# Optimization experiments

Measured on AMD Instinct MI355X. Metric: run time of the kernel, lower is better.

The kernel has to match this reference:

```python
import jax, jax.numpy as jnp
import numpy as np

DIM = 1024
E = 8
K = 2
EPS = 1e-5

def _ln(x, g, b):
    mu = jnp.mean(x, axis=-1, keepdims=True)
    var = jnp.mean(jnp.square(x - mu), axis=-1, keepdims=True)
    return (x - mu) * jax.lax.rsqrt(var + EPS) * g + b

def setup_inputs() -> dict:
    key = jax.random.key(0)
    ks = jax.random.split(key, 8)
    H = 2 * DIM
    s_in = 1.0 / np.sqrt(DIM)
    s_h = 1.0 / np.sqrt(H)
    return {
        "x": jax.random.normal(ks[0], (2, 2048, DIM), dtype=jnp.float32),
        "gate_w": jax.random.uniform(ks[1], (DIM, E), minval=-s_in, maxval=s_in, dtype=jnp.float32),
        "w1": jax.random.uniform(ks[2], (E, DIM, H), minval=-s_in, maxval=s_in, dtype=jnp.float32),
        "b1": jax.random.uniform(ks[3], (E, H), minval=-s_in, maxval=s_in, dtype=jnp.float32),
        "ln1_g": jnp.ones((E, H), dtype=jnp.float32),
        "ln1_b": jnp.zeros((E, H), dtype=jnp.float32),
        "w2": jax.random.uniform(ks[4], (E, H, DIM), minval=-s_h, maxval=s_h, dtype=jnp.float32),
        "b2": jax.random.uniform(ks[5], (E, DIM), minval=-s_h, maxval=s_h, dtype=jnp.float32),
        "ln_g": jnp.ones((DIM,), dtype=jnp.float32),
        "ln_b": jnp.zeros((DIM,), dtype=jnp.float32),
    }

def reference(x, gate_w, w1, b1, ln1_g, ln1_b, w2, b2, ln_g, ln_b):
    shape = x.shape
    xf = x.reshape(-1, shape[-1])                      # [T, D]
    gates = jax.nn.softmax(xf @ gate_w, axis=-1)       # [T, E]
    topw, topi = jax.lax.top_k(gates, K)               # [T, K]
    topw = topw / jnp.sum(topw, axis=-1, keepdims=True)
    # combine weights per expert: [T, E]
    combine = jnp.sum(topw[:, :, None] * jax.nn.one_hot(topi, E, dtype=xf.dtype), axis=1)
    # run all experts on all tokens (vectorized grouped GEMM), combine by gate mask
    h = jnp.einsum('td,edh->teh', xf, w1) + b1          # [T, E, 2D]
    h = _ln(h, ln1_g, ln1_b)
    h = jax.nn.gelu(h, approximate=False)
    y = jnp.einsum('teh,ehd->ted', h, w2) + b2          # [T, E, D]
    out = jnp.einsum('ted,te->td', y, combine)          # [T, D]
    out = _ln(out + xf, ln_g, ln_b)
    return out.reshape(shape)
```

## Files before the change

kernel.cpp:

```cpp
#include <hip/hip_runtime.h>
#include <hip/hip_bf16.h>

#define DIMX 1024
#define HID  2048
#define NE   8
#define NT   4096
#define NPAIR 8192
#define MAXSTRIP 72

typedef __attribute__((ext_vector_type(8))) __bf16 bf16x8;
typedef __attribute__((ext_vector_type(4))) float f32x4;

__device__ inline unsigned short f2bf(float f) {
  union { float f; unsigned u; } v; v.f = f;
  unsigned r = v.u + 0x7FFFu + ((v.u >> 16) & 1u);
  return (unsigned short)(r >> 16);
}
__device__ inline float bf2f(unsigned short h) {
  union { unsigned u; float f; } v; v.u = ((unsigned)h) << 16;
  return v.f;
}

__device__ __forceinline__ void gload_lds16(const unsigned short* g, unsigned short* l) {
  __builtin_amdgcn_global_load_lds(
      (const __attribute__((address_space(1))) unsigned int*)g,
      (__attribute__((address_space(3))) unsigned int*)l, 16, 0, 0);
}

#define O_CNT   0u
#define O_TOK   1024u
#define O_TK    132096u
#define O_PW    263168u
#define O_TI    394240u
#define O_TW    427008u
#define O_POFF  459776u
#define O_SE    459904u
#define O_SR0   460416u
#define O_XBF   524288u
#define O_W1T   16777216u
#define O_W2T   50331648u
#define O_H     83886080u
#define O_Y     121634816u

__global__ __launch_bounds__(256) void k_gate_cvt(const float* __restrict__ x,
                                                  const float* __restrict__ gw,
                                                  unsigned short* __restrict__ xbf,
                                                  int* __restrict__ ti,
                                                  float* __restrict__ tw) {
  int t = blockIdx.x * 4 + (threadIdx.x >> 6);
  int lane = threadIdx.x & 63;
  const float4* xr = (const float4*)(x + (size_t)t * DIMX);
  ushort4* xo = (ushort4*)(xbf + (size_t)t * DIMX);
  float p[NE];
#pragma unroll
  for (int e = 0; e < NE; e++) p[e] = 0.f;
#pragma unroll
  for (int j = 0; j < 4; j++) {
    int idx4 = j * 64 + lane;
    float4 v = xr[idx4];
    ushort4 o; o.x = f2bf(v.x); o.y = f2bf(v.y); o.z = f2bf(v.z); o.w = f2bf(v.w);
    xo[idx4] = o;
    const float4* gp = (const float4*)(gw + (size_t)(idx4 * 4) * NE);
    float4 gA = gp[0], gB = gp[1], gC = gp[2], gD = gp[3];
    float4 gE = gp[4], gF = gp[5], gG = gp[6], gH = gp[7];
    p[0] += v.x * gA.x + v.y * gC.x + v.z * gE.x + v.w * gG.x;
    p[1] += v.x * gA.y + v.y * gC.y + v.z * gE.y + v.w * gG.y;
    p[2] += v.x * gA.z + v.y * gC.z + v.z * gE.z + v.w * gG.z;
    p[3] += v.x * gA.w + v.y * gC.w + v.z * gE.w + v.w * gG.w;
    p[4] += v.x * gB.x + v.y * gD.x + v.z * gF.x + v.w * gH.x;
    p[5] += v.x * gB.y + v.y * gD.y + v.z * gF.y + v.w * gH.y;
    p[6] += v.x * gB.z + v.y * gD.z + v.z * gF.z + v.w * gH.z;
    p[7] += v.x * gB.w + v.y * gD.w + v.z * gF.w + v.w * gH.w;
  }
#pragma unroll
  for (int e = 0; e < NE; e++)
#pragma unroll
    for (int off = 32; off > 0; off >>= 1) p[e] += __shfl_xor(p[e], off);
  if (lane == 0) {
    int ia = 0; float va = p[0];
#pragma unroll
    for (int e = 1; e < NE; e++) if (p[e] > va) { va = p[e]; ia = e; }
    int ib = -1; float vb = -3.0e38f;
#pragma unroll
    for (int e = 0; e < NE; e++) { if (e == ia) continue; if (p[e] > vb) { vb = p[e]; ib = e; } }
    float w0 = 1.f / (1.f + expf(vb - va));
    ti[t * 2] = ia;     tw[t * 2] = w0;
    ti[t * 2 + 1] = ib; tw[t * 2 + 1] = 1.f - w0;
  }
}

__global__ __launch_bounds__(512) void k_build(const int* __restrict__ ti,
                                               const float* __restrict__ tw,
                                               int* __restrict__ cnt,
                                               int* __restrict__ poffs,
                                               int* __restrict__ s_e, int* __restrict__ s_r0,
                                               int* __restrict__ ptok, int* __restrict__ ptk,
                                               float* __restrict__ pw) {
  __shared__ int sti[NPAIR];
  __shared__ float stw[NPAIR];
  __shared__ int scnt[NE];
  for (int i = threadIdx.x; i < NPAIR; i += 512) { sti[i] = ti[i]; stw[i] = tw[i]; }
  __syncthreads();
  int wid = threadIdx.x >> 6;
  int lane = threadIdx.x & 63;
  int c = 0;
  for (int p = lane; p < NPAIR; p += 64) c += (sti[p] == wid) ? 1 : 0;
#pragma unroll
  for (int off = 32; off > 0; off >>= 1) c += __shfl_xor(c, off);
  if (lane == 0) scnt[wid] = c;
  __syncthreads();
  if (threadIdx.x == 0) {
    int s = 0, pacc = 0;
    for (int e = 0; e < NE; e++) {
      cnt[e] = scnt[e];
      poffs[e] = pacc;
      int ns = (scnt[e] + 127) >> 7;
      for (int k = 0; k < ns; k++) { s_e[s] = e; s_r0[s] = k * 128; s++; }
      pacc += ns * 128;
    }
    poffs[NE] = pacc;
    for (; s < MAXSTRIP; s++) { s_e[s] = -1; s_r0[s] = 0; }
  }
  int base = 0;
  for (int p0 = 0; p0 < NPAIR; p0 += 64) {
    int p = p0 + lane;
    bool m = (sti[p] == wid);
    unsigned long long mask = __ballot(m);
    if (m) {
      int pos = base + __popcll(mask & ((1ull << lane) - 1ull));
      ptok[wid * NT + pos] = p >> 1;
      ptk[wid * NT + pos] = p;
      pw[wid * NT + pos] = stw[p];
    }
    base += __popcll(mask);
  }
}

__global__ __launch_bounds__(256) void k_transpose_cvt(const float* __restrict__ in,
                                                       unsigned short* __restrict__ out,
                                                       int R, int C) {
  __shared__ float tile[64][73];
  int e = blockIdx.z;
  const float* ip = in + (size_t)e * R * C;
  unsigned short* op = out + (size_t)e * R * C;
  int c0 = blockIdx.x * 64, r0 = blockIdx.y * 64;
  int tx = threadIdx.x & 15, ty = threadIdx.x >> 4;
#pragma unroll
  for (int i = 0; i < 4; i++) {
    int row = ty + i * 16;
    float4 v = *(const float4*)(ip + (size_t)(r0 + row) * C + c0 + tx * 4);
    tile[row][tx * 4] = v.x; tile[row][tx * 4 + 1] = v.y;
    tile[row][tx * 4 + 2] = v.z; tile[row][tx * 4 + 3] = v.w;
  }
  __syncthreads();
  int rx = threadIdx.x & 15, cy = threadIdx.x >> 4;
  int r_off = rx * 4;
#pragma unroll
  for (int i = 0; i < 4; i++) {
    int cc = cy + i * 16;
    ushort4 h;
    h.x = f2bf(tile[r_off][cc]);     h.y = f2bf(tile[r_off + 1][cc]);
    h.z = f2bf(tile[r_off + 2][cc]); h.w = f2bf(tile[r_off + 3][cc]);
    *(ushort4*)(op + (size_t)(c0 + cc) * R + r0 + r_off) = h;
  }
}

#define BM 128
#define BN 128
#define BK 32

__global__ __launch_bounds__(256) void k_gemm1(
    const unsigned short* __restrict__ xbf,
    const unsigned short* __restrict__ w1t,
    const float* __restrict__ bias1,
    const int* __restrict__ cnt, const int* __restrict__ s_e,
    const int* __restrict__ s_r0, const int* __restrict__ poffs,
    const int* __restrict__ ptok,
    unsigned short* __restrict__ hpre)
{
  int lid = blockIdx.x + 16 * blockIdx.y;
  int xcd = lid & 7;
  int t4 = lid >> 3;
  int colb = t4 & 15;
  int s = xcd * 9 + (t4 >> 4);
  int e = s_e[s];
  if (e < 0) return;
  int r0e = s_r0[s];
  int n_e = cnt[e];
  int pbase = poffs[e];
  int col0 = colb * BN;

  __shared__ __align__(16) unsigned short As[2][BM][BK];
  __shared__ __align__(16) unsigned short Bs[2][BN][BK];

  int tid = threadIdx.x;
  int lane = tid & 63, wid = tid >> 6;
  int wr = wid >> 1, wc = wid & 1;
  int quad = lane >> 4, m16 = lane & 15;

  int rr = lane >> 2;
  int csrc = ((lane & 3) ^ ((lane >> 3) & 3)) * 8;
  int ga0 = r0e + wid * 32 + rr;      if (ga0 >= n_e) ga0 = n_e - 1;
  int ga1 = r0e + wid * 32 + 16 + rr; if (ga1 >= n_e) ga1 = n_e - 1;
  int t0 = ptok[e * NT + ga0];
  int t1 = ptok[e * NT + ga1];
  const unsigned short* a0p = xbf + (size_t)t0 * DIMX + csrc;
  const unsigned short* a1p = xbf + (size_t)t1 * DIMX + csrc;
  const unsigned short* bbase = w1t + (size_t)e * HID * DIMX;
  const unsigned short* b0p = bbase + (size_t)(col0 + wid * 32 + rr) * DIMX + csrc;
  const unsigned short* b1p = bbase + (size_t)(col0 + wid * 32 + 16 + rr) * DIMX + csrc;

  int ca = (quad ^ ((m16 >> 1) & 3)) * 8;

  f32x4 acc[4][4];
#pragma unroll
  for (int i = 0; i < 4; i++)
#pragma unroll
    for (int j = 0; j < 4; j++) acc[i][j] = (f32x4)(0.f);

#define STAGE1(b, kk) do { \
    gload_lds16(a0p + (kk), &As[b][wid * 32][0]); \
    gload_lds16(a1p + (kk), &As[b][wid * 32 + 16][0]); \
    gload_lds16(b0p + (kk), &Bs[b][wid * 32][0]); \
    gload_lds16(b1p + (kk), &Bs[b][wid * 32 + 16][0]); \
  } while (0)

  STAGE1(0, 0);
  __syncthreads();
  int cur = 0;
  for (int k0 = 0; k0 < DIMX; k0 += BK) {
    if (k0 + BK < DIMX) STAGE1(cur ^ 1, k0 + BK);
    bf16x8 af[4], bfr[4];
#pragma unroll
    for (int i = 0; i < 4; i++) af[i]  = *(const bf16x8*)&As[cur][wr * 64 + i * 16 + m16][ca];
#pragma unroll
    for (int j = 0; j < 4; j++) bfr[j] = *(const bf16x8*)&Bs[cur][wc * 64 + j * 16 + m16][ca];
#pragma unroll
    for (int i = 0; i < 4; i++)
#pragma unroll
      for (int j = 0; j < 4; j++)
        acc[i][j] = __builtin_amdgcn_mfma_f32_16x16x32_bf16(af[i], bfr[j], acc[i][j], 0, 0, 0);
    __syncthreads();
    cur ^= 1;
  }
#undef STAGE1

  float bj[4];
#pragma unroll
  for (int j = 0; j < 4; j++) bj[j] = bias1[e * HID + col0 + wc * 64 + j * 16 + m16];
#pragma unroll
  for (int i = 0; i < 4; i++) {
#pragma unroll
    for (int r = 0; r < 4; r++) {
      int g = r0e + wr * 64 + i * 16 + quad * 4 + r;
      if (g < n_e) {
        size_t rowbase = (size_t)(pbase + g) * HID;
#pragma unroll
        for (int j = 0; j < 4; j++) {
          int colg = col0 + wc * 64 + j * 16 + m16;
          hpre[rowbase + colg] = f2bf(acc[i][j][r] + bj[j]);
        }
      }
    }
  }
}

__global__ __launch_bounds__(256) void k_ln_gelu(unsigned short* __restrict__ h,
                                                 const float* __restrict__ g1,
                                                 const float* __restrict__ bb1,
                                                 const int* __restrict__ s_e) {
  int row = blockIdx.x * 4 + (threadIdx.x >> 6);
  int e = s_e[row >> 7];
  if (e < 0) return;
  int lane = threadIdx.x & 63;
  unsigned short* p = h + (size_t)row * HID;
  int4* p4 = (int4*)p;
  int4 raw[4];
#pragma unroll
  for (int sg = 0; sg < 4; sg++) raw[sg] = p4[sg * 64 + lane];
  float v[32];
#pragma unroll
  for (int sg = 0; sg < 4; sg++) {
    const unsigned short* u = (const unsigned short*)&raw[sg];
#pragma unroll
    for (int k = 0; k < 8; k++) v[sg * 8 + k] = bf2f(u[k]);
  }
  float s = 0.f;
#pragma unroll
  for (int i = 0; i < 32; i++) s += v[i];
#pragma unroll
  for (int off = 32; off > 0; off >>= 1) s += __shfl_xor(s, off);
  float mean = s * (1.f / HID);
  float sq = 0.f;
#pragma unroll
  for (int i = 0; i < 32; i++) { float d = v[i] - mean; sq += d * d; }
#pragma unroll
  for (int off = 32; off > 0; off >>= 1) sq += __shfl_xor(sq, off);
  float rstd = rsqrtf(sq * (1.f / HID) + 1e-5f);
  const float4* gg = (const float4*)(g1 + (size_t)e * HID);
  const float4* gb = (const float4*)(bb1 + (size_t)e * HID);
#pragma unroll
  for (int sg = 0; sg < 4; sg++) {
    float4 ga = gg[sg * 128 + lane * 2], gc = gg[sg * 128 + lane * 2 + 1];
    float4 ba = gb[sg * 128 + lane * 2], bc = gb[sg * 128 + lane * 2 + 1];
    float gn[8] = {ga.x, ga.y, ga.z, ga.w, gc.x, gc.y, gc.z, gc.w};
    float bn[8] = {ba.x, ba.y, ba.z, ba.w, bc.x, bc.y, bc.z, bc.w};
    unsigned short o[8];
#pragma unroll
    for (int k = 0; k < 8; k++) {
      float xn = (v[sg * 8 + k] - mean) * rstd * gn[k] + bn[k];
      float ge = 0.5f * xn * (1.f + erff(xn * 0.7071067811865476f));
      o[k] = f2bf(ge);
    }
    p4[sg * 64 + lane] = *(const int4*)o;
  }
}

__global__ __launch_bounds__(256) void k_gemm2(
    const unsigned short* __restrict__ hb,
    const unsigned short* __restrict__ w2t,
    const float* __restrict__ bias2,
    const int* __restrict__ cnt, const int* __restrict__ s_e,
    const int* __restrict__ s_r0, const int* __restrict__ poffs,
    const int* __restrict__ ptk, const float* __restrict__ pw,
    float* __restrict__ ybufA, float* __restrict__ ybufB)
{
  int lid = blockIdx.x + 8 * (blockIdx.y + 72 * blockIdx.z);
  int xcd = lid & 7;
  int t4 = lid >> 3;
  int colb = t4 & 7;
  int rem = t4 >> 3;
  int ks = rem & 1;
  int s = xcd * 9 + (rem >> 1);
  int e = s_e[s];
  if (e < 0) return;
  int r0e = s_r0[s];
  int n_e = cnt[e];
  int pbase = poffs[e];
  int col0 = colb * BN;
  int kbase = ks << 10;

  __shared__ __align__(16) unsigned short As[2][BM][BK];
  __shared__ __align__(16) unsigned short Bs[2][BN][BK];

  int tid = threadIdx.x;
  int lane = tid & 63, wid = tid >> 6;
  int wr = wid >> 1, wc = wid & 1;
  int quad = lane >> 4, m16 = lane & 15;

  int rr = lane >> 2;
  int csrc = ((lane & 3) ^ ((lane >> 3) & 3)) * 8;
  int ga0 = r0e + wid * 32 + rr;      if (ga0 >= n_e) ga0 = n_e - 1;
  int ga1 = r0e + wid * 32 + 16 + rr; if (ga1 >= n_e) ga1 = n_e - 1;
  const unsigned short* a0p = hb + (size_t)(pbase + ga0) * HID + kbase + csrc;
  const unsigned short* a1p = hb + (size_t)(pbase + ga1) * HID + kbase + csrc;
  const unsigned short* bbase = w2t + (size_t)e * DIMX * HID;
  const unsigned short* b0p = bbase + (size_t)(col0 + wid * 32 + rr) * HID + kbase + csrc;
  const unsigned short* b1p = bbase + (size_t)(col0 + wid * 32 + 16 + rr) * HID + kbase + csrc;

  int ca = (quad ^ ((m16 >> 1) & 3)) * 8;

  f32x4 acc[4][4];
#pragma unroll
  for (int i = 0; i < 4; i++)
#pragma unroll
    for (int j = 0; j < 4; j++) acc[i][j] = (f32x4)(0.f);

#define STAGE2(b, kk) do { \
    gload_lds16(a0p + (kk), &As[b][wid * 32][0]); \
    gload_lds16(a1p + (kk), &As[b][wid * 32 + 16][0]); \
    gload_lds16(b0p + (kk), &Bs[b][wid * 32][0]); \
    gload_lds16(b1p + (kk), &Bs[b][wid * 32 + 16][0]); \
  } while (0)

  STAGE2(0, 0);
  __syncthreads();
  int cur = 0;
  for (int k0 = 0; k0 < HID / 2; k0 += BK) {
    if (k0 + BK < HID / 2) STAGE2(cur ^ 1, k0 + BK);
    bf16x8 af[4], bfr[4];
#pragma unroll
    for (int i = 0; i < 4; i++) af[i]  = *(const bf16x8*)&As[cur][wr * 64 + i * 16 + m16][ca];
#pragma unroll
    for (int j = 0; j < 4; j++) bfr[j] = *(const bf16x8*)&Bs[cur][wc * 64 + j * 16 + m16][ca];
#pragma unroll
    for (int i = 0; i < 4; i++)
#pragma unroll
      for (int j = 0; j < 4; j++)
        acc[i][j] = __builtin_amdgcn_mfma_f32_16x16x32_bf16(af[i], bfr[j], acc[i][j], 0, 0, 0);
    __syncthreads();
    cur ^= 1;
  }
#undef STAGE2

  float* yb = ks ? ybufB : ybufA;
  float bj[4];
#pragma unroll
  for (int j = 0; j < 4; j++)
    bj[j] = ks ? bias2[e * DIMX + col0 + wc * 64 + j * 16 + m16] : 0.f;
#pragma unroll
  for (int i = 0; i < 4; i++) {
#pragma unroll
    for (int r = 0; r < 4; r++) {
      int g = r0e + wr * 64 + i * 16 + quad * 4 + r;
      if (g < n_e) {
        int pi = e * NT + g;
        float w = pw[pi];
        size_t obase = (size_t)ptk[pi] * DIMX;
#pragma unroll
        for (int j = 0; j < 4; j++) {
          int colg = col0 + wc * 64 + j * 16 + m16;
          yb[obase + colg] = (acc[i][j][r] + bj[j]) * w;
        }
      }
    }
  }
}

__global__ __launch_bounds__(256) void k_final(const float* __restrict__ ybA,
                                               const float* __restrict__ ybB,
                                               const float* __restrict__ x,
                                               const float* __restrict__ lg,
                                               const float* __restrict__ lb,
                                               float* __restrict__ out) {
  int t = blockIdx.x * 4 + (threadIdx.x >> 6);
  int lane = threadIdx.x & 63;
  const float4* yA0 = (const float4*)(ybA + (size_t)t * 2 * DIMX);
  const float4* yA1 = yA0 + DIMX / 4;
  const float4* yB0 = (const float4*)(ybB + (size_t)t * 2 * DIMX);
  const float4* yB1 = yB0 + DIMX / 4;
  const float4* x4 = (const float4*)(x + (size_t)t * DIMX);
  float4 v[4];
  float s = 0.f;
#pragma unroll
  for (int sg = 0; sg < 4; sg++) {
    int idx = sg * 64 + lane;
    float4 a = yA0[idx], b = yA1[idx], a2 = yB0[idx], b2 = yB1[idx], c = x4[idx];
    v[sg].x = a.x + b.x + a2.x + b2.x + c.x;
    v[sg].y = a.y + b.y + a2.y + b2.y + c.y;
    v[sg].z = a.z + b.z + a2.z + b2.z + c.z;
    v[sg].w = a.w + b.w + a2.w + b2.w + c.w;
    s += v[sg].x + v[sg].y + v[sg].z + v[sg].w;
  }
#pragma unroll
  for (int off = 32; off > 0; off >>= 1) s += __shfl_xor(s, off);
  float mean = s * (1.f / DIMX);
  float sq = 0.f;
#pragma unroll
  for (int sg = 0; sg < 4; sg++) {
    float dx = v[sg].x - mean, dy = v[sg].y - mean, dz = v[sg].z - mean, dw = v[sg].w - mean;
    sq += dx * dx + dy * dy + dz * dz + dw * dw;
  }
#pragma unroll
  for (int off = 32; off > 0; off >>= 1) sq += __shfl_xor(sq, off);
  float rstd = rsqrtf(sq * (1.f / DIMX) + 1e-5f);
  float4* o4 = (float4*)(out + (size_t)t * DIMX);
#pragma unroll
  for (int sg = 0; sg < 4; sg++) {
    int idx = sg * 64 + lane;
    float4 g = ((const float4*)lg)[idx], bb = ((const float4*)lb)[idx];
    float4 o;
    o.x = (v[sg].x - mean) * rstd * g.x + bb.x;
    o.y = (v[sg].y - mean) * rstd * g.y + bb.y;
    o.z = (v[sg].z - mean) * rstd * g.z + bb.z;
    o.w = (v[sg].w - mean) * rstd * g.w + bb.w;
    o4[idx] = o;
  }
}

extern "C" void kernel_launch(void* const* d_in, const int* in_sizes, int n_in,
                              void* d_out, int out_size, void* d_ws, size_t ws_size,
                              hipStream_t stream) {
  const float* x     = (const float*)d_in[0];
  const float* gw    = (const float*)d_in[1];
  const float* w1    = (const float*)d_in[2];
  const float* b1    = (const float*)d_in[3];
  const float* ln1g  = (const float*)d_in[4];
  const float* ln1b  = (const float*)d_in[5];
  const float* w2    = (const float*)d_in[6];
  const float* b2    = (const float*)d_in[7];
  const float* lng   = (const float*)d_in[8];
  const float* lnb   = (const float*)d_in[9];
  float* out = (float*)d_out;

  char* ws = (char*)d_ws;
  int* cnt   = (int*)(ws + O_CNT);
  int* ptok  = (int*)(ws + O_TOK);
  int* ptk   = (int*)(ws + O_TK);
  float* pw  = (float*)(ws + O_PW);
  int* ti    = (int*)(ws + O_TI);
  float* tw  = (float*)(ws + O_TW);
  int* poffs = (int*)(ws + O_POFF);
  int* s_e   = (int*)(ws + O_SE);
  int* s_r0  = (int*)(ws + O_SR0);
  unsigned short* xbf  = (unsigned short*)(ws + O_XBF);
  unsigned short* w1t  = (unsigned short*)(ws + O_W1T);
  unsigned short* w2t  = (unsigned short*)(ws + O_W2T);
  unsigned short* hpre = (unsigned short*)(ws + O_H);
  float* ybufA = (float*)(ws + O_Y);
  float* ybufB = (float*)(ws + O_W1T);

  hipLaunchKernelGGL(k_gate_cvt, dim3(NT / 4), dim3(256), 0, stream, x, gw, xbf, ti, tw);
  hipLaunchKernelGGL(k_build, dim3(1), dim3(512), 0, stream, ti, tw, cnt, poffs, s_e, s_r0,
                     ptok, ptk, pw);
  hipLaunchKernelGGL(k_transpose_cvt, dim3(HID / 64, DIMX / 64, NE), dim3(256), 0, stream,
                     w1, w1t, DIMX, HID);
  hipLaunchKernelGGL(k_transpose_cvt, dim3(DIMX / 64, HID / 64, NE), dim3(256), 0, stream,
                     w2, w2t, HID, DIMX);
  hipLaunchKernelGGL(k_gemm1, dim3(HID / BN, MAXSTRIP), dim3(256), 0, stream,
                     xbf, w1t, b1, cnt, s_e, s_r0, poffs, ptok, hpre);
  hipLaunchKernelGGL(k_ln_gelu, dim3(MAXSTRIP * BM / 4), dim3(256), 0, stream,
                     hpre, ln1g, ln1b, s_e);
  hipLaunchKernelGGL(k_gemm2, dim3(DIMX / BN, MAXSTRIP, 2), dim3(256), 0, stream,
                     hpre, w2t, b2, cnt, s_e, s_r0, poffs, ptk, pw, ybufA, ybufB);
  hipLaunchKernelGGL(k_final, dim3(NT / 4), dim3(256), 0, stream, ybufA, ybufB, x, lng, lnb, out);
}
```

Measured before the change: 385.9 us.

## Triple-buffer LDS in both expert GEMMs with explicit vmcnt waits

```diff
diff --git a/kernel.cpp b/kernel.cpp
--- a/kernel.cpp
+++ b/kernel.cpp
@@ -168,6 +168,8 @@
 #define BM 128
 #define BN 128
 #define BK 32
+
+#define KSTEPS 32
 
 __global__ __launch_bounds__(256) void k_gemm1(
     const unsigned short* __restrict__ xbf,
@@ -190,8 +192,8 @@
   int pbase = poffs[e];
   int col0 = colb * BN;
 
-  __shared__ __align__(16) unsigned short As[2][BM][BK];
-  __shared__ __align__(16) unsigned short Bs[2][BN][BK];
+  __shared__ __align__(16) unsigned short As[3][BM][BK];
+  __shared__ __align__(16) unsigned short Bs[3][BN][BK];
 
   int tid = threadIdx.x;
   int lane = tid & 63, wid = tid >> 6;
@@ -226,10 +228,23 @@
   } while (0)
 
   STAGE1(0, 0);
-  __syncthreads();
-  int cur = 0;
-  for (int k0 = 0; k0 < DIMX; k0 += BK) {
-    if (k0 + BK < DIMX) STAGE1(cur ^ 1, k0 + BK);
+  STAGE1(1, BK);
+  int cur = 0, pb = 2;
+  for (int k = 0; k < KSTEPS; ++k) {
+    asm volatile("s_waitcnt lgkmcnt(0)" ::: "memory");
+    __builtin_amdgcn_sched_barrier(0);
+    __builtin_amdgcn_s_barrier();
+    if (k + 2 < KSTEPS) {
+      STAGE1(pb, (k + 2) * BK);
+      asm volatile("s_waitcnt vmcnt(8)" ::: "memory");
+    } else if (k + 2 == KSTEPS) {
+      asm volatile("s_waitcnt vmcnt(4)" ::: "memory");
+    } else {
+      asm volatile("s_waitcnt vmcnt(0)" ::: "memory");
+    }
+    __builtin_amdgcn_sched_barrier(0);
+    __builtin_amdgcn_s_barrier();
+    __builtin_amdgcn_sched_barrier(0);
     bf16x8 af[4], bfr[4];
 #pragma unroll
     for (int i = 0; i < 4; i++) af[i]  = *(const bf16x8*)&As[cur][wr * 64 + i * 16 + m16][ca];
@@ -240,8 +255,8 @@
 #pragma unroll
       for (int j = 0; j < 4; j++)
         acc[i][j] = __builtin_amdgcn_mfma_f32_16x16x32_bf16(af[i], bfr[j], acc[i][j], 0, 0, 0);
-    __syncthreads();
-    cur ^= 1;
+    cur = (cur == 2) ? 0 : cur + 1;
+    pb  = (pb == 2) ? 0 : pb + 1;
   }
 #undef STAGE1
 
@@ -340,8 +355,8 @@
   int col0 = colb * BN;
   int kbase = ks << 10;
 
-  __shared__ __align__(16) unsigned short As[2][BM][BK];
-  __shared__ __align__(16) unsigned short Bs[2][BN][BK];
+  __shared__ __align__(16) unsigned short As[3][BM][BK];
+  __shared__ __align__(16) unsigned short Bs[3][BN][BK];
 
   int tid = threadIdx.x;
   int lane = tid & 63, wid = tid >> 6;
@@ -374,10 +389,23 @@
   } while (0)
 
   STAGE2(0, 0);
-  __syncthreads();
-  int cur = 0;
-  for (int k0 = 0; k0 < HID / 2; k0 += BK) {
-    if (k0 + BK < HID / 2) STAGE2(cur ^ 1, k0 + BK);
+  STAGE2(1, BK);
+  int cur = 0, pb = 2;
+  for (int k = 0; k < KSTEPS; ++k) {
+    asm volatile("s_waitcnt lgkmcnt(0)" ::: "memory");
+    __builtin_amdgcn_sched_barrier(0);
+    __builtin_amdgcn_s_barrier();
+    if (k + 2 < KSTEPS) {
+      STAGE2(pb, (k + 2) * BK);
+      asm volatile("s_waitcnt vmcnt(8)" ::: "memory");
+    } else if (k + 2 == KSTEPS) {
+      asm volatile("s_waitcnt vmcnt(4)" ::: "memory");
+    } else {
+      asm volatile("s_waitcnt vmcnt(0)" ::: "memory");
+    }
+    __builtin_amdgcn_sched_barrier(0);
+    __builtin_amdgcn_s_barrier();
+    __builtin_amdgcn_sched_barrier(0);
     bf16x8 af[4], bfr[4];
 #pragma unroll
     for (int i = 0; i < 4; i++) af[i]  = *(const bf16x8*)&As[cur][wr * 64 + i * 16 + m16][ca];
@@ -388,8 +416,8 @@
 #pragma unroll
       for (int j = 0; j < 4; j++)
         acc[i][j] = __builtin_amdgcn_mfma_f32_16x16x32_bf16(af[i], bfr[j], acc[i][j], 0, 0, 0);
-    __syncthreads();
-    cur ^= 1;
+    cur = (cur == 2) ? 0 : cur + 1;
+    pb  = (pb == 2) ? 0 : pb + 1;
   }
 #undef STAGE2
 
```

Result: faster. 373.6 us (-3.2%).
